# Optimization experiments

Hardware: AMD Instinct MI355X
Metric: run time of the kernel (lower is better)

The kernel has to match this reference:

```python
import jax, jax.numpy as jnp
import numpy as np
import math

B, S, D_MODEL, H = 2, 2048, 1024, 16
HD = D_MODEL // H  # head_dim = 64


def _rope(x, seq_len):
    # x: [B, S, H, HD]; standard rotate-half RoPE with base 10000
    d = x.shape[-1]
    inv_freq = 1.0 / (10000.0 ** (jnp.arange(0, d, 2, dtype=jnp.float32) / d))
    t = jnp.arange(seq_len, dtype=jnp.float32)
    freqs = t[:, None] * inv_freq[None, :]              # [S, HD/2]
    emb = jnp.concatenate([freqs, freqs], axis=-1)      # [S, HD]
    cos = jnp.cos(emb)[None, :, None, :]
    sin = jnp.sin(emb)[None, :, None, :]
    x1, x2 = jnp.split(x, 2, axis=-1)
    rot = jnp.concatenate([-x2, x1], axis=-1)
    return x * cos + rot * sin


def setup_inputs() -> dict:
    key = jax.random.key(0)
    ks = jax.random.split(key, 11)
    s = 1.0 / math.sqrt(D_MODEL)
    return {
        "query": jax.random.normal(ks[0], (B, S, D_MODEL), jnp.float32),
        "keys": jax.random.normal(ks[1], (B, S, D_MODEL), jnp.float32),
        "values": jax.random.normal(ks[2], (B, S, D_MODEL), jnp.float32),
        "Wq": jax.random.normal(ks[3], (D_MODEL, D_MODEL), jnp.float32) * s,
        "bq": jnp.zeros((D_MODEL,), jnp.float32),
        "Wk": jax.random.normal(ks[4], (D_MODEL, D_MODEL), jnp.float32) * s,
        "bk": jnp.zeros((D_MODEL,), jnp.float32),
        "Wv": jax.random.normal(ks[5], (D_MODEL, D_MODEL), jnp.float32) * s,
        "bv": jnp.zeros((D_MODEL,), jnp.float32),
        "Wo": jax.random.normal(ks[6], (D_MODEL, D_MODEL), jnp.float32) * s,
        "bo": jnp.zeros((D_MODEL,), jnp.float32),
    }


def reference(query, keys, values, Wq, bq, Wk, bk, Wv, bv, Wo, bo):
    b, s, _ = query.shape
    scale = math.sqrt(HD)
    q = (query @ Wq.T + bq).reshape(b, s, H, HD)   # [B,S,H,HD]
    k = (keys @ Wk.T + bk).reshape(b, s, H, HD)
    v = (values @ Wv.T + bv).reshape(b, s, H, HD)
    q = _rope(q, s)
    k = _rope(k, s)
    # scores: [B,H,Sq,Sk]
    scores = jnp.einsum('bqhd,bkhd->bhqk', q, k)
    causal = jnp.tril(jnp.ones((s, s), dtype=bool))[None, None]
    scores = jnp.where(causal, scores, -jnp.inf) / scale
    attn = jax.nn.softmax(scores, axis=-1)
    ctx = jnp.einsum('bhqk,bkhd->bqhd', attn, v).reshape(b, s, H * HD)
    out = ctx @ Wo.T + bo
    return out, attn
```

## Files before the change

### kernel.cpp

```cpp
#include <hip/hip_runtime.h>
#include <hip/hip_bf16.h>
#include <stdint.h>
#include <math.h>


typedef __attribute__((ext_vector_type(8))) __bf16 bf16x8;
typedef __attribute__((ext_vector_type(4))) float f32x4;

__device__ __forceinline__ unsigned short f2bf(float f) {
  unsigned int u = __float_as_uint(f);
  u += 0x7fffu + ((u >> 16) & 1u);
  return (unsigned short)(u >> 16);
}

typedef const __attribute__((address_space(1))) unsigned int* gas_ptr;
typedef __attribute__((address_space(3))) unsigned int* las_ptr;
__device__ __forceinline__ void glds16(const void* g, void* l) {
  __builtin_amdgcn_global_load_lds((gas_ptr)g, (las_ptr)l, 16, 0, 0);
}

__global__ __launch_bounds__(256) void cvt_all(
    const float* __restrict__ a0, const float* __restrict__ a1,
    const float* __restrict__ a2, const float* __restrict__ w0,
    const float* __restrict__ w1, const float* __restrict__ w2,
    const float* __restrict__ w3, unsigned short* __restrict__ ws,
    float2* __restrict__ rtab) {
  const int z = blockIdx.z;
  if (z == 7) {
    const int i = blockIdx.x * 256 + threadIdx.x;
    if (i < 65536) {
      const int spos = i >> 5, d = i & 31;
      const double invf = pow(10000.0, -(double)d / 32.0);
      double sn, cs;
      sincos((double)spos * invf, &sn, &cs);
      rtab[i] = make_float2((float)cs, (float)sn);
    }
    return;
  }
  const float* src;
  unsigned short* dst;
  int n;
  if (z == 0)      { src = a0; dst = ws;             n = 4194304; }
  else if (z == 1) { src = a1; dst = ws + 4194304;   n = 4194304; }
  else if (z == 2) { src = a2; dst = ws + 8388608;   n = 4194304; }
  else if (z == 3) { src = w0; dst = ws + 12582912;  n = 1048576; }
  else if (z == 4) { src = w1; dst = ws + 13631488;  n = 1048576; }
  else if (z == 5) { src = w2; dst = ws + 14680064;  n = 1048576; }
  else             { src = w3; dst = ws + 15728640;  n = 1048576; }
  const int n4 = n >> 2;
  for (int i = blockIdx.x * 256 + threadIdx.x; i < n4; i += gridDim.x * 256) {
    float4 f = ((const float4*)src)[i];
    ushort4 u;
    u.x = f2bf(f.x); u.y = f2bf(f.y); u.z = f2bf(f.z); u.w = f2bf(f.w);
    ((ushort4*)dst)[i] = u;
  }
}

__global__ __launch_bounds__(256) void gemm_qkv(
    const unsigned short* __restrict__ xq, const unsigned short* __restrict__ xk,
    const unsigned short* __restrict__ xv, const unsigned short* __restrict__ wq,
    const unsigned short* __restrict__ wk, const unsigned short* __restrict__ wv,
    const float* __restrict__ bq, const float* __restrict__ bk,
    const float* __restrict__ bv, const float2* __restrict__ rtab,
    unsigned short* __restrict__ qo, unsigned short* __restrict__ ko,
    unsigned short* __restrict__ vo) {
  const int z = blockIdx.z;
  const unsigned short* A = (z == 0) ? xq : (z == 1) ? xk : xv;
  const unsigned short* W = (z == 0) ? wq : (z == 1) ? wk : wv;
  const float* bias = (z == 0) ? bq : (z == 1) ? bk : bv;
  unsigned short* out = (z == 0) ? qo : (z == 1) ? ko : vo;

  const int t = threadIdx.x;
  const int lane = t & 63, wave = t >> 6;
  const int wr = wave >> 1, wc = wave & 1;
  const int lrow = lane & 15, lkb = lane >> 4;
  const int m0 = blockIdx.y * 128, n0 = blockIdx.x * 128;

  __shared__ __align__(16) unsigned short abuf[8192];
  __shared__ __align__(16) unsigned short bbuf[8192];

  f32x4 acc[4][4] = {};

  for (int k0 = 0; k0 < 1024; k0 += 64) {
    __syncthreads();
#pragma unroll
    for (int i = 0; i < 4; ++i) {
      int slot = i * 256 + t;
      int kb = slot >> 7, row = slot & 127;
      glds16(A + (size_t)(m0 + row) * 1024 + k0 + kb * 8, &abuf[slot * 8]);
      glds16(W + (size_t)(n0 + row) * 1024 + k0 + kb * 8, &bbuf[slot * 8]);
    }
    __syncthreads();
#pragma unroll
    for (int ks = 0; ks < 2; ++ks) {
      bf16x8 af[4], bfr[4];
#pragma unroll
      for (int mi = 0; mi < 4; ++mi)
        af[mi] = *(const bf16x8*)&abuf[((ks * 4 + lkb) * 128 + wr * 64 + mi * 16 + lrow) * 8];
#pragma unroll
      for (int ni = 0; ni < 4; ++ni)
        bfr[ni] = *(const bf16x8*)&bbuf[((ks * 4 + lkb) * 128 + wc * 64 + ni * 16 + lrow) * 8];
#pragma unroll
      for (int mi = 0; mi < 4; ++mi)
#pragma unroll
        for (int ni = 0; ni < 4; ++ni)
          acc[mi][ni] = __builtin_amdgcn_mfma_f32_16x16x32_bf16(af[mi], bfr[ni],
                                                                acc[mi][ni], 0, 0, 0);
    }
  }

  const int nbase = n0 + wc * 64;
  float bias_v[4];
#pragma unroll
  for (int ni = 0; ni < 4; ++ni) bias_v[ni] = bias[nbase + ni * 16 + lrow];

  const int mbase = m0 + wr * 64 + 4 * lkb;
  const bool rope = (z < 2);
  const float qsc = (z == 0) ? 0.125f : 1.0f;

#pragma unroll
  for (int mi = 0; mi < 4; ++mi) {
#pragma unroll
    for (int r = 0; r < 4; ++r) {
      const int m = mbase + mi * 16 + r;
      const int bidx = m >> 11, spos = m & 2047;
      float vals[4];
#pragma unroll
      for (int ni = 0; ni < 4; ++ni) vals[ni] = acc[mi][ni][r] + bias_v[ni];
      if (rope) {
#pragma unroll
        for (int ni = 0; ni < 2; ++ni) {
          const int d = ni * 16 + lrow;
          const float2 cs2 = rtab[spos * 32 + d];
          float x1 = vals[ni], x2 = vals[ni + 2];
          vals[ni] = (x1 * cs2.x - x2 * cs2.y) * qsc;
          vals[ni + 2] = (x2 * cs2.x + x1 * cs2.y) * qsc;
        }
      }
#pragma unroll
      for (int ni = 0; ni < 4; ++ni) {
        const int n = nbase + ni * 16 + lrow;
        const int h = n >> 6, d = n & 63;
        out[(size_t)((bidx * 16 + h) * 2048 + spos) * 64 + d] = f2bf(vals[ni]);
      }
    }
  }
}

__global__ __launch_bounds__(256) void gemm_out(
    const unsigned short* __restrict__ A, const unsigned short* __restrict__ W,
    const float* __restrict__ bias, float* __restrict__ out) {
  const int t = threadIdx.x;
  const int lane = t & 63, wave = t >> 6;
  const int wr = wave >> 1, wc = wave & 1;
  const int lrow = lane & 15, lkb = lane >> 4;
  const int m0 = blockIdx.y * 128, n0 = blockIdx.x * 128;

  __shared__ __align__(16) unsigned short abuf[8192];
  __shared__ __align__(16) unsigned short bbuf[8192];

  f32x4 acc[4][4] = {};

  for (int k0 = 0; k0 < 1024; k0 += 64) {
    __syncthreads();
#pragma unroll
    for (int i = 0; i < 4; ++i) {
      int slot = i * 256 + t;
      int kb = slot >> 7, row = slot & 127;
      glds16(A + (size_t)(m0 + row) * 1024 + k0 + kb * 8, &abuf[slot * 8]);
      glds16(W + (size_t)(n0 + row) * 1024 + k0 + kb * 8, &bbuf[slot * 8]);
    }
    __syncthreads();
#pragma unroll
    for (int ks = 0; ks < 2; ++ks) {
      bf16x8 af[4], bfr[4];
#pragma unroll
      for (int mi = 0; mi < 4; ++mi)
        af[mi] = *(const bf16x8*)&abuf[((ks * 4 + lkb) * 128 + wr * 64 + mi * 16 + lrow) * 8];
#pragma unroll
      for (int ni = 0; ni < 4; ++ni)
        bfr[ni] = *(const bf16x8*)&bbuf[((ks * 4 + lkb) * 128 + wc * 64 + ni * 16 + lrow) * 8];
#pragma unroll
      for (int mi = 0; mi < 4; ++mi)
#pragma unroll
        for (int ni = 0; ni < 4; ++ni)
          acc[mi][ni] = __builtin_amdgcn_mfma_f32_16x16x32_bf16(af[mi], bfr[ni],
                                                                acc[mi][ni], 0, 0, 0);
    }
  }

  const int nbase = n0 + wc * 64;
  float bias_v[4];
#pragma unroll
  for (int ni = 0; ni < 4; ++ni) bias_v[ni] = bias[nbase + ni * 16 + lrow];
  const int mbase = m0 + wr * 64 + 4 * lkb;
#pragma unroll
  for (int mi = 0; mi < 4; ++mi)
#pragma unroll
    for (int r = 0; r < 4; ++r) {
      const int m = mbase + mi * 16 + r;
      float* orow = out + (size_t)m * 1024 + nbase;
#pragma unroll
      for (int ni = 0; ni < 4; ++ni)
        orow[ni * 16 + lrow] = acc[mi][ni][r] + bias_v[ni];
    }
}

__global__ __launch_bounds__(256) void transpose_v(
    const unsigned short* __restrict__ v, unsigned short* __restrict__ vt) {
  const int s0 = blockIdx.x * 64;
  const int bh = blockIdx.y;
  __shared__ __align__(16) unsigned short tile[64][80];
  const int t = threadIdx.x;
  {
    const int row = t >> 2, cb = t & 3;
    const unsigned short* src = v + (size_t)(bh * 2048 + s0 + row) * 64 + cb * 16;
    *(uint4*)&tile[row][cb * 16] = *(const uint4*)src;
    *(uint4*)&tile[row][cb * 16 + 8] = *(const uint4*)(src + 8);
  }
  __syncthreads();
  {
    const int d = t >> 2, sc = t & 3;
    __align__(16) unsigned short tmp[16];
#pragma unroll
    for (int u = 0; u < 16; ++u) tmp[u] = tile[sc * 16 + u][d];
    unsigned short* dst = vt + (size_t)(bh * 64 + d) * 2048 + s0 + sc * 16;
    *(uint4*)dst = *(const uint4*)&tmp[0];
    *(uint4*)(dst + 8) = *(const uint4*)&tmp[8];
  }
}

__global__ __launch_bounds__(256) void attn_kernel(
    const unsigned short* __restrict__ Q, const unsigned short* __restrict__ Km,
    const unsigned short* __restrict__ Vt, float* __restrict__ attn,
    unsigned short* __restrict__ ctx) {
  const int p = blockIdx.x;
  const int qta = p, qtb = 31 - p;
  const int bh = blockIdx.y;
  const int t = threadIdx.x;
  const int lane = t & 63, wave = t >> 6;
  const int lrow = lane & 15, lg = lane >> 4;
  const int wq0a = qta * 64 + wave * 16;
  const int wq0b = qtb * 64 + wave * 16;

  const unsigned short* Qb = Q + (size_t)bh * 2048 * 64;
  const unsigned short* Kb = Km + (size_t)bh * 2048 * 64;
  const unsigned short* Vb = Vt + (size_t)bh * 64 * 2048;
  float* attn_b = attn + (size_t)bh * 2048 * 2048;

  __shared__ __align__(16) unsigned short kbuf[4096];
  __shared__ __align__(16) unsigned short vbuf[4096];
  __shared__ __align__(16) unsigned short pbuf[4][1024];

  bf16x8 qfa[2], qfb[2];
#pragma unroll
  for (int dk = 0; dk < 2; ++dk) {
    qfa[dk] = *(const bf16x8*)(Qb + (size_t)(wq0a + lrow) * 64 + dk * 32 + lg * 8);
    qfb[dk] = *(const bf16x8*)(Qb + (size_t)(wq0b + lrow) * 64 + dk * 32 + lg * 8);
  }

  float l_a[4] = {0.f, 0.f, 0.f, 0.f};
  float l_b[4] = {0.f, 0.f, 0.f, 0.f};

  auto lupdate = [&](const unsigned short* buf, int kbase, int wq0,
                     const bf16x8* qf, float* l_loc) {
    f32x4 s[4] = {};
#pragma unroll
    for (int fc = 0; fc < 4; ++fc)
#pragma unroll
      for (int dk = 0; dk < 2; ++dk) {
        bf16x8 kf = *(const bf16x8*)&buf[((dk * 4 + lg) * 64 + fc * 16 + lrow) * 8];
        s[fc] = __builtin_amdgcn_mfma_f32_16x16x32_bf16(qf[dk], kf, s[fc], 0, 0, 0);
      }
#pragma unroll
    for (int r = 0; r < 4; ++r) {
      const int qg = wq0 + 4 * lg + r;
      float sum = 0.f;
#pragma unroll
      for (int fc = 0; fc < 4; ++fc) {
        const int kg = kbase + fc * 16 + lrow;
        sum += __expf((kg <= qg) ? s[fc][r] : -1e30f);
      }
      l_loc[r] += sum;
    }
  };

  for (int kt = 0; kt <= qtb; kt += 2) {
    const int k0 = kt * 64;
    const bool two = (kt + 1) <= qtb;
    __syncthreads();
#pragma unroll
    for (int i = 0; i < 2; ++i) {
      int slot = i * 256 + t;
      int cb = slot >> 6, row = slot & 63;
      glds16(Kb + (size_t)(k0 + row) * 64 + cb * 8, &kbuf[slot * 8]);
      if (two)
        glds16(Kb + (size_t)(k0 + 64 + row) * 64 + cb * 8, &vbuf[slot * 8]);
    }
    __syncthreads();
    if (kt <= qta) lupdate(kbuf, k0, wq0a, qfa, l_a);
    lupdate(kbuf, k0, wq0b, qfb, l_b);
    if (two) {
      if (kt + 1 <= qta) lupdate(vbuf, k0 + 64, wq0a, qfa, l_a);
      lupdate(vbuf, k0 + 64, wq0b, qfb, l_b);
    }
  }

  float loglinva[4], loglinvb[4];
#pragma unroll
  for (int r = 0; r < 4; ++r) {
    float la = l_a[r], lb = l_b[r];
#pragma unroll
    for (int off = 1; off < 16; off <<= 1) {
      la += __shfl_xor(la, off);
      lb += __shfl_xor(lb, off);
    }
    loglinva[r] = -__logf(la);
    loglinvb[r] = -__logf(lb);
  }

  f32x4 oaa[4] = {};
  f32x4 oab[4] = {};

  auto process = [&](int k0, int wq0, const bf16x8* qf, const float* loglinv,
                     f32x4* oa) {
    f32x4 s[4] = {};
#pragma unroll
    for (int fc = 0; fc < 4; ++fc)
#pragma unroll
      for (int dk = 0; dk < 2; ++dk) {
        bf16x8 kf = *(const bf16x8*)&kbuf[((dk * 4 + lg) * 64 + fc * 16 + lrow) * 8];
        s[fc] = __builtin_amdgcn_mfma_f32_16x16x32_bf16(qf[dk], kf, s[fc], 0, 0, 0);
      }
#pragma unroll
    for (int r = 0; r < 4; ++r) {
      const int qg = wq0 + 4 * lg + r;
      const int q_ = 4 * lg + r;
      float* arow = attn_b + (size_t)qg * 2048 + k0;
#pragma unroll
      for (int fc = 0; fc < 4; ++fc) {
        const int kg = k0 + fc * 16 + lrow;
        const float pv = (kg <= qg) ? __expf(s[fc][r] + loglinv[r]) : 0.f;
        arow[fc * 16 + lrow] = pv;
        const int k_ = fc * 16 + lrow;
        const int dl = q_ + 16 * ((k_ >> 3) & 3);
        const int kk = k_ >> 5, j = k_ & 7;
        int byteo = (kk * 64 + dl) * 16 + j * 2;
        byteo ^= ((kk * 8 + (dl >> 3)) & 7) << 4;
        *(unsigned short*)((char*)pbuf[wave] + byteo) = f2bf(pv);
      }
    }
#pragma unroll
    for (int kk = 0; kk < 2; ++kk) {
      int rbyte = (kk * 64 + lane) * 16;
      rbyte ^= ((kk * 8 + (lane >> 3)) & 7) << 4;
      bf16x8 pa = *(const bf16x8*)((char*)pbuf[wave] + rbyte);
#pragma unroll
      for (int fd = 0; fd < 4; ++fd) {
        bf16x8 vf = *(const bf16x8*)&vbuf[((kk * 4 + lg) * 64 + fd * 16 + lrow) * 8];
        oa[fd] = __builtin_amdgcn_mfma_f32_16x16x32_bf16(pa, vf, oa[fd], 0, 0, 0);
      }
    }
  };

  for (int kt = 0; kt <= qtb; ++kt) {
    const int k0 = kt * 64;
    __syncthreads();
#pragma unroll
    for (int i = 0; i < 2; ++i) {
      int slot = i * 256 + t;
      int cb = slot >> 6, row = slot & 63;
      glds16(Kb + (size_t)(k0 + row) * 64 + cb * 8, &kbuf[slot * 8]);
      glds16(Vb + (size_t)row * 2048 + k0 + cb * 8, &vbuf[slot * 8]);
    }
    __syncthreads();
    if (kt <= qta) process(k0, wq0a, qfa, loglinva, oaa);
    process(k0, wq0b, qfb, loglinvb, oab);
  }

  {
    const int zc0a = (qta + 1) * 16;
    for (int rr = 0; rr < 16; ++rr) {
      float4* arow = (float4*)(attn_b + (size_t)(wq0a + rr) * 2048);
      for (int c = zc0a + lane; c < 512; c += 64)
        arow[c] = make_float4(0.f, 0.f, 0.f, 0.f);
    }
    const int zc0b = (qtb + 1) * 16;
    for (int rr = 0; rr < 16; ++rr) {
      float4* arow = (float4*)(attn_b + (size_t)(wq0b + rr) * 2048);
      for (int c = zc0b + lane; c < 512; c += 64)
        arow[c] = make_float4(0.f, 0.f, 0.f, 0.f);
    }
  }

  const int bidx = bh >> 4, h = bh & 15;
#pragma unroll
  for (int fd = 0; fd < 4; ++fd)
#pragma unroll
    for (int r = 0; r < 4; ++r) {
      const int qga = wq0a + 4 * lg + r;
      const int qgb = wq0b + 4 * lg + r;
      ctx[(size_t)(bidx * 2048 + qga) * 1024 + h * 64 + fd * 16 + lrow] =
          f2bf(oaa[fd][r]);
      ctx[(size_t)(bidx * 2048 + qgb) * 1024 + h * 64 + fd * 16 + lrow] =
          f2bf(oab[fd][r]);
    }
}

extern "C" void kernel_launch(void* const* d_in, const int* in_sizes, int n_in,
                              void* d_out, int out_size, void* d_ws, size_t ws_size,
                              hipStream_t stream) {
  const float* q_in = (const float*)d_in[0];
  const float* k_in = (const float*)d_in[1];
  const float* v_in = (const float*)d_in[2];
  const float* Wq = (const float*)d_in[3];
  const float* bq = (const float*)d_in[4];
  const float* Wk = (const float*)d_in[5];
  const float* bk = (const float*)d_in[6];
  const float* Wv = (const float*)d_in[7];
  const float* bv = (const float*)d_in[8];
  const float* Wo = (const float*)d_in[9];
  const float* bo = (const float*)d_in[10];

  unsigned short* ws = (unsigned short*)d_ws;
  float* outp = (float*)d_out;

  const size_t OXQ = 0, OXK = 4194304, OXV = 8388608;
  const size_t OWQ = 12582912, OWK = 13631488, OWV = 14680064, OWO = 15728640;
  const size_t OQ = 16777216, OK = 20971520, OV = 25165824;
  const size_t OTAB = 29360128;
  const size_t OVT = OXK;
  const size_t OCTX = OXQ;
  float2* rtab = (float2*)(ws + OTAB);

  cvt_all<<<dim3(512, 1, 8), 256, 0, stream>>>(q_in, k_in, v_in, Wq, Wk, Wv, Wo,
                                               ws, rtab);
  gemm_qkv<<<dim3(8, 32, 3), 256, 0, stream>>>(ws + OXQ, ws + OXK, ws + OXV,
                                               ws + OWQ, ws + OWK, ws + OWV,
                                               bq, bk, bv, rtab,
                                               ws + OQ, ws + OK, ws + OV);
  transpose_v<<<dim3(32, 32), 256, 0, stream>>>(ws + OV, ws + OVT);
  attn_kernel<<<dim3(16, 32), 256, 0, stream>>>(ws + OQ, ws + OK, ws + OVT,
                                                outp + 4194304, ws + OCTX);
  gemm_out<<<dim3(8, 32), 256, 0, stream>>>(ws + OCTX, ws + OWO, bo, outp);
}
```

Measured before the change: 305.4 us.

## Load K and V fragments directly from global memory instead of LDS staging

```diff
diff --git a/kernel.cpp b/kernel.cpp
--- a/kernel.cpp
+++ b/kernel.cpp
@@ -248,8 +248,6 @@
   const unsigned short* Vb = Vt + (size_t)bh * 64 * 2048;
   float* attn_b = attn + (size_t)bh * 2048 * 2048;
 
-  __shared__ __align__(16) unsigned short kbuf[4096];
-  __shared__ __align__(16) unsigned short vbuf[4096];
   __shared__ __align__(16) unsigned short pbuf[4][1024];
 
   bf16x8 qfa[2], qfb[2];
@@ -262,47 +260,54 @@
   float l_a[4] = {0.f, 0.f, 0.f, 0.f};
   float l_b[4] = {0.f, 0.f, 0.f, 0.f};
 
-  auto lupdate = [&](const unsigned short* buf, int kbase, int wq0,
-                     const bf16x8* qf, float* l_loc) {
-    f32x4 s[4] = {};
+  for (int kt = 0; kt <= qtb; ++kt) {
+    const int k0 = kt * 64;
+    bf16x8 kf[4][2];
 #pragma unroll
     for (int fc = 0; fc < 4; ++fc)
 #pragma unroll
-      for (int dk = 0; dk < 2; ++dk) {
-        bf16x8 kf = *(const bf16x8*)&buf[((dk * 4 + lg) * 64 + fc * 16 + lrow) * 8];
-        s[fc] = __builtin_amdgcn_mfma_f32_16x16x32_bf16(qf[dk], kf, s[fc], 0, 0, 0);
-      }
-#pragma unroll
-    for (int r = 0; r < 4; ++r) {
-      const int qg = wq0 + 4 * lg + r;
-      float sum = 0.f;
-#pragma unroll
-      for (int fc = 0; fc < 4; ++fc) {
-        const int kg = kbase + fc * 16 + lrow;
-        sum += __expf((kg <= qg) ? s[fc][r] : -1e30f);
-      }
-      l_loc[r] += sum;
-    }
-  };
-
-  for (int kt = 0; kt <= qtb; kt += 2) {
-    const int k0 = kt * 64;
-    const bool two = (kt + 1) <= qtb;
-    __syncthreads();
-#pragma unroll
-    for (int i = 0; i < 2; ++i) {
-      int slot = i * 256 + t;
-      int cb = slot >> 6, row = slot & 63;
-      glds16(Kb + (size_t)(k0 + row) * 64 + cb * 8, &kbuf[slot * 8]);
-      if (two)
-        glds16(Kb + (size_t)(k0 + 64 + row) * 64 + cb * 8, &vbuf[slot * 8]);
-    }
-    __syncthreads();
-    if (kt <= qta) lupdate(kbuf, k0, wq0a, qfa, l_a);
-    lupdate(kbuf, k0, wq0b, qfb, l_b);
-    if (two) {
-      if (kt + 1 <= qta) lupdate(vbuf, k0 + 64, wq0a, qfa, l_a);
-      lupdate(vbuf, k0 + 64, wq0b, qfb, l_b);
+      for (int dk = 0; dk < 2; ++dk)
+        kf[fc][dk] = *(const bf16x8*)(Kb + (size_t)(k0 + fc * 16 + lrow) * 64 +
+                                      (dk * 4 + lg) * 8);
+    {
+      f32x4 s[4] = {};
+#pragma unroll
+      for (int fc = 0; fc < 4; ++fc)
+#pragma unroll
+        for (int dk = 0; dk < 2; ++dk)
+          s[fc] = __builtin_amdgcn_mfma_f32_16x16x32_bf16(qfb[dk], kf[fc][dk],
+                                                          s[fc], 0, 0, 0);
+#pragma unroll
+      for (int r = 0; r < 4; ++r) {
+        const int qg = wq0b + 4 * lg + r;
+        float sum = 0.f;
+#pragma unroll
+        for (int fc = 0; fc < 4; ++fc) {
+          const int kg = k0 + fc * 16 + lrow;
+          sum += __expf((kg <= qg) ? s[fc][r] : -1e30f);
+        }
+        l_b[r] += sum;
+      }
+    }
+    if (kt <= qta) {
+      f32x4 s[4] = {};
+#pragma unroll
+      for (int fc = 0; fc < 4; ++fc)
+#pragma unroll
+        for (int dk = 0; dk < 2; ++dk)
+          s[fc] = __builtin_amdgcn_mfma_f32_16x16x32_bf16(qfa[dk], kf[fc][dk],
+                                                          s[fc], 0, 0, 0);
+#pragma unroll
+      for (int r = 0; r < 4; ++r) {
+        const int qg = wq0a + 4 * lg + r;
+        float sum = 0.f;
+#pragma unroll
+        for (int fc = 0; fc < 4; ++fc) {
+          const int kg = k0 + fc * 16 + lrow;
+          sum += __expf((kg <= qg) ? s[fc][r] : -1e30f);
+        }
+        l_a[r] += sum;
+      }
     }
   }
 
@@ -322,16 +327,15 @@
   f32x4 oaa[4] = {};
   f32x4 oab[4] = {};
 
-  auto process = [&](int k0, int wq0, const bf16x8* qf, const float* loglinv,
-                     f32x4* oa) {
+  auto process = [&](int k0, int wq0, const bf16x8* qf, const bf16x8 (*kf)[2],
+                     const float* loglinv, f32x4* oa) {
     f32x4 s[4] = {};
 #pragma unroll
     for (int fc = 0; fc < 4; ++fc)
 #pragma unroll
-      for (int dk = 0; dk < 2; ++dk) {
-        bf16x8 kf = *(const bf16x8*)&kbuf[((dk * 4 + lg) * 64 + fc * 16 + lrow) * 8];
-        s[fc] = __builtin_amdgcn_mfma_f32_16x16x32_bf16(qf[dk], kf, s[fc], 0, 0, 0);
-      }
+      for (int dk = 0; dk < 2; ++dk)
+        s[fc] = __builtin_amdgcn_mfma_f32_16x16x32_bf16(qf[dk], kf[fc][dk],
+                                                        s[fc], 0, 0, 0);
 #pragma unroll
     for (int r = 0; r < 4; ++r) {
       const int qg = wq0 + 4 * lg + r;
@@ -357,7 +361,8 @@
       bf16x8 pa = *(const bf16x8*)((char*)pbuf[wave] + rbyte);
 #pragma unroll
       for (int fd = 0; fd < 4; ++fd) {
-        bf16x8 vf = *(const bf16x8*)&vbuf[((kk * 4 + lg) * 64 + fd * 16 + lrow) * 8];
+        bf16x8 vf = *(const bf16x8*)(Vb + (size_t)(fd * 16 + lrow) * 2048 + k0 +
+                                     (kk * 4 + lg) * 8);
         oa[fd] = __builtin_amdgcn_mfma_f32_16x16x32_bf16(pa, vf, oa[fd], 0, 0, 0);
       }
     }
@@ -365,17 +370,15 @@
 
   for (int kt = 0; kt <= qtb; ++kt) {
     const int k0 = kt * 64;
-    __syncthreads();
-#pragma unroll
-    for (int i = 0; i < 2; ++i) {
-      int slot = i * 256 + t;
-      int cb = slot >> 6, row = slot & 63;
-      glds16(Kb + (size_t)(k0 + row) * 64 + cb * 8, &kbuf[slot * 8]);
-      glds16(Vb + (size_t)row * 2048 + k0 + cb * 8, &vbuf[slot * 8]);
-    }
-    __syncthreads();
-    if (kt <= qta) process(k0, wq0a, qfa, loglinva, oaa);
-    process(k0, wq0b, qfb, loglinvb, oab);
+    bf16x8 kf[4][2];
+#pragma unroll
+    for (int fc = 0; fc < 4; ++fc)
+#pragma unroll
+      for (int dk = 0; dk < 2; ++dk)
+        kf[fc][dk] = *(const bf16x8*)(Kb + (size_t)(k0 + fc * 16 + lrow) * 64 +
+                                      (dk * 4 + lg) * 8);
+    if (kt <= qta) process(k0, wq0a, qfa, kf, loglinva, oaa);
+    process(k0, wq0b, qfb, kf, loglinvb, oab);
   }
 
   {
```

Result: slower. 380.7 us (+24.7%).
